# Kernel optimization log

Hardware: AMD Instinct MI355X
Metric: run time of the kernel (lower is better)

The kernel has to match this reference:

```python
import jax, jax.numpy as jnp
import numpy as np

IN_DIM, INTER_DIM, OUT_DIM = 512, 256, 512


def setup_inputs() -> dict:
    key = jax.random.key(0)
    k1, k2, k3, k4 = jax.random.split(key, 4)
    feat_map = jax.random.normal(k1, (8, IN_DIM, 64, 64), dtype=jnp.float32)
    # xavier-uniform-style init scales
    lim_p = float(np.sqrt(6.0 / (IN_DIM + INTER_DIM)))
    lim_w = float(np.sqrt(6.0 / (IN_DIM + OUT_DIM)))
    phi_w = jax.random.uniform(k2, (INTER_DIM, IN_DIM), jnp.float32, -lim_p, lim_p)
    theta_w = jax.random.uniform(k3, (INTER_DIM, IN_DIM), jnp.float32, -lim_p, lim_p)
    weight = jax.random.uniform(k4, (IN_DIM, OUT_DIM), jnp.float32, -lim_w, lim_w)
    return {"feat_map": feat_map, "phi_w": phi_w, "theta_w": theta_w, "weight": weight}


def reference(feat_map, phi_w, theta_w, weight):
    B, D, H, W = feat_map.shape
    # b c h w -> b (h w) c
    feat_vec = jnp.transpose(feat_map.reshape(B, D, H * W), (0, 2, 1))  # [B, HW, D]
    phi = jnp.einsum('bnc,ic->bni', feat_vec, phi_w)      # [B, HW, inter]
    theta = jnp.einsum('bnc,ic->bni', feat_vec, theta_w)  # [B, HW, inter]
    product = jnp.einsum('bni,bmi->bnm', phi, theta)      # [B, HW, HW]
    phi_norm = jnp.linalg.norm(phi, axis=-1, keepdims=True)      # [B, HW, 1]
    theta_norm = jnp.linalg.norm(theta, axis=-1, keepdims=True)  # [B, HW, 1]
    norms = phi_norm * jnp.transpose(theta_norm, (0, 2, 1))      # [B, HW, HW]
    sim = jax.nn.softmax(product / norms, axis=-1)
    out = jnp.einsum('bnm,bmc->bnc', sim, feat_vec)  # [B, HW, D]
    out = jnp.einsum('bnc,cd->bnd', out, weight)     # [B, HW, out_dim]
    # b (h w) d -> b d h w
    updated = jnp.transpose(out, (0, 2, 1)).reshape(B, -1, H, W)
    return jax.nn.relu(updated)
```

## Files before the change

kernel.cpp:

```cpp
#include <hip/hip_runtime.h>


typedef short s8v __attribute__((ext_vector_type(8)));
typedef float f4v __attribute__((ext_vector_type(4)));

__device__ inline ushort f2bf(float x) {
  union { float f; unsigned u; } v; v.f = x;
  unsigned u = v.u + 0x7fff + ((v.u >> 16) & 1);
  return (ushort)(u >> 16);
}

__global__ __launch_bounds__(256) void k0a(const float* __restrict__ feat,
                                           ushort* __restrict__ featT,
                                           ushort* __restrict__ featV) {
  int bid = blockIdx.x;
  int b = bid >> 9, cb = (bid >> 6) & 7, mt = bid & 63;
  int t = threadIdx.x;
  __shared__ ushort tile[64][72];

#pragma unroll
  for (int p = 0; p < 4; p++) {
    int ci = p * 16 + (t >> 4);
    int mi = (t & 15) * 4;
    float4 v = *(const float4*)&feat[((size_t)(b * 512 + cb * 64 + ci)) * 4096 + mt * 64 + mi];
    ushort4 u; u.x = f2bf(v.x); u.y = f2bf(v.y); u.z = f2bf(v.z); u.w = f2bf(v.w);
    *(ushort4*)&featV[((size_t)(b * 64 + mt) * 512 + cb * 64 + ci) * 64 + mi] = u;
    tile[ci][mi] = u.x; tile[ci][mi + 1] = u.y; tile[ci][mi + 2] = u.z; tile[ci][mi + 3] = u.w;
  }
  __syncthreads();
  int m = t >> 2, cs = (t & 3) * 16;
  ushort tmp[16];
#pragma unroll
  for (int j = 0; j < 16; j++) tmp[j] = tile[cs + j][m];
  ushort* dst = &featT[((size_t)(b * 4096 + mt * 64 + m)) * 512 + cb * 64 + cs];
  *(s8v*)dst = *(s8v*)&tmp[0];
  *(s8v*)(dst + 8) = *(s8v*)&tmp[8];
}

__global__ __launch_bounds__(256) void k0b(const float* __restrict__ pw,
                                           const float* __restrict__ tw,
                                           ushort* __restrict__ wbp,
                                           ushort* __restrict__ wbt) {
  int bid = blockIdx.x;
  const float* src = (bid < 128) ? pw : tw;
  ushort* dst = (bid < 128) ? wbp : wbt;
  int idx = ((bid & 127) * 256 + threadIdx.x) * 4;
  float4 v = *(const float4*)&src[idx];
  ushort4 u; u.x = f2bf(v.x); u.y = f2bf(v.y); u.z = f2bf(v.z); u.w = f2bf(v.w);
  *(ushort4*)&dst[idx] = u;
}

__global__ __launch_bounds__(256) void k0c(const float* __restrict__ w,
                                           ushort* __restrict__ wT) {
  int bid = blockIdx.x;
  int cb = bid >> 3, db = bid & 7;
  int t = threadIdx.x;
  __shared__ ushort tile[64][72];
#pragma unroll
  for (int p = 0; p < 4; p++) {
    int ci = p * 16 + (t >> 4);
    int di = (t & 15) * 4;
    float4 v = *(const float4*)&w[(size_t)(cb * 64 + ci) * 512 + db * 64 + di];
    tile[ci][di] = f2bf(v.x); tile[ci][di + 1] = f2bf(v.y);
    tile[ci][di + 2] = f2bf(v.z); tile[ci][di + 3] = f2bf(v.w);
  }
  __syncthreads();
  int d = t >> 2, cs = (t & 3) * 16;
  ushort tmp[16];
#pragma unroll
  for (int j = 0; j < 16; j++) tmp[j] = tile[cs + j][d];
  ushort* dst = &wT[(size_t)(db * 64 + d) * 512 + cb * 64 + cs];
  *(s8v*)dst = *(s8v*)&tmp[0];
  *(s8v*)(dst + 8) = *(s8v*)&tmp[8];
}

__global__ __launch_bounds__(512) void k1_gemm(
    const ushort* __restrict__ featT, const ushort* __restrict__ wbp,
    const ushort* __restrict__ wbt, ushort* __restrict__ phi_n,
    ushort* __restrict__ theta_n) {
  int bid = blockIdx.x;
  int b = bid & 7;
  int rest = bid >> 3;
  int half = rest & 1;
  int nt = rest >> 1;
  const ushort* wb = half ? wbt : wbp;
  ushort* dst = half ? theta_n : phi_n;
  int t = threadIdx.x;
  int lane = t & 63, w = t >> 6;
  int col = lane & 15, quad = lane >> 4;
  int n0 = nt * 128;

  const ushort* abase =
      featT + ((size_t)(b * 4096 + n0 + w * 16 + col)) * 512 + quad * 8;

  f4v acc[16];
#pragma unroll
  for (int i = 0; i < 16; i++) acc[i] = (f4v){0.f, 0.f, 0.f, 0.f};

#pragma unroll 2
  for (int kc = 0; kc < 16; kc++) {
    s8v a = *(const s8v*)(abase + kc * 32);
#pragma unroll
    for (int it = 0; it < 16; it++) {
      s8v bf = *(const s8v*)(wb + (size_t)(it * 16 + col) * 512 + kc * 32 + quad * 8);
      acc[it] = __builtin_amdgcn_mfma_f32_16x16x32_bf16(a, bf, acc[it], 0, 0, 0);
    }
  }
  float rinv[4];
#pragma unroll
  for (int reg = 0; reg < 4; reg++) {
    float ss = 0.f;
#pragma unroll
    for (int it = 0; it < 16; it++) ss += acc[it][reg] * acc[it][reg];
    ss += __shfl_xor(ss, 1); ss += __shfl_xor(ss, 2);
    ss += __shfl_xor(ss, 4); ss += __shfl_xor(ss, 8);
    rinv[reg] = rsqrtf(ss);
  }
#pragma unroll
  for (int it = 0; it < 16; it++) {
#pragma unroll
    for (int reg = 0; reg < 4; reg++) {
      dst[((size_t)(b * 4096 + n0 + w * 16 + quad * 4 + reg)) * 256 + it * 16 + col] =
          f2bf(acc[it][reg] * rinv[reg]);
    }
  }
}

__global__ __launch_bounds__(512, 2) void k3_attn(
    const ushort* __restrict__ phi_n, const ushort* __restrict__ theta_n,
    const ushort* __restrict__ featV, ushort* __restrict__ out1) {
  int bid = blockIdx.x;
  int b = bid & 7;
  int n0 = (bid >> 3) << 6;
  int t = threadIdx.x;
  int lane = t & 63, w = t >> 6;
  int col = lane & 15, quad = lane >> 4;
  int mh4 = w & 3, rh = w >> 2;
  int l32 = lane & 31, h32 = lane >> 5;
  int cs = col & 7;

  __shared__ __align__(16) ushort ks[2 * 16384];
  __shared__ __align__(16) ushort ps[2 * 4096];
  __shared__ float dred[4 * 64];

  s8v qfA[8], qfB[8];
  {
    const ushort* qa = phi_n + ((size_t)(b * 4096 + n0 + rh * 32 + col)) * 256 + quad * 8;
#pragma unroll
    for (int f = 0; f < 8; f++) qfA[f] = *(const s8v*)(qa + f * 32);
    const ushort* qb = qa + 16 * 256;
#pragma unroll
    for (int f = 0; f < 8; f++) qfB[f] = *(const s8v*)(qb + f * 32);
  }

  const ushort* thb = theta_n + (size_t)b * 4096 * 256;
  const ushort* vbb = featV + (size_t)b * 64 * 512 * 64 + (size_t)(w * 64) * 64;

  f4v acc[16];
#pragma unroll
  for (int i = 0; i < 16; i++) acc[i] = (f4v){0.f, 0.f, 0.f, 0.f};
  float denp[8] = {0.f, 0.f, 0.f, 0.f, 0.f, 0.f, 0.f, 0.f};

#pragma unroll
  for (int u = 0; u < 4; u++) {
    int row = w * 8 + u * 2 + h32;
    s8v val = *(const s8v*)(thb + (size_t)row * 256 + l32 * 8);
    *(s8v*)(ks + row * 256 + ((l32 ^ (row & 7)) * 8)) = val;
  }
  __syncthreads();

#pragma unroll 1
  for (int mt = 0; mt < 64; mt++) {
    const ushort* kc_ = ks + (mt & 1) * 16384;
    ushort* kn_ = ks + ((mt & 1) ^ 1) * 16384;
    ushort* pw_ = ps + (mt & 1) * 4096;

    s8v kreg[4];
    if (mt < 63) {
      int m1 = (mt + 1) << 6;
#pragma unroll
      for (int u = 0; u < 4; u++) {
        int row = w * 8 + u * 2 + h32;
        kreg[u] = *(const s8v*)(thb + (size_t)(m1 + row) * 256 + l32 * 8);
      }
    }
    s8v v0[4], v1[4];
    {
      const ushort* vb = vbb + (size_t)mt * 32768;
#pragma unroll
      for (int ct = 0; ct < 4; ct++) {
        const ushort* p = vb + (ct * 16 + col) * 64 + quad * 8;
        v0[ct] = *(const s8v*)p;
        v1[ct] = *(const s8v*)(p + 32);
      }
    }

    f4v svA = (f4v){0.f, 0.f, 0.f, 0.f};
    f4v svB = (f4v){0.f, 0.f, 0.f, 0.f};
    {
      const ushort* kb = kc_ + (mh4 * 16 + col) * 256;
      __builtin_amdgcn_s_setprio(1);
#pragma unroll
      for (int kk = 0; kk < 8; kk++) {
        int pos = ((kk * 4 + quad) ^ cs) * 8;
        s8v bf = *(const s8v*)(kb + pos);
        svA = __builtin_amdgcn_mfma_f32_16x16x32_bf16(qfA[kk], bf, svA, 0, 0, 0);
        svB = __builtin_amdgcn_mfma_f32_16x16x32_bf16(qfB[kk], bf, svB, 0, 0, 0);
      }
      __builtin_amdgcn_s_setprio(0);
    }

    float pA[4], pB[4];
#pragma unroll
    for (int r = 0; r < 4; r++) {
      pA[r] = __expf(svA[r]);
      pB[r] = __expf(svB[r]);
      denp[r] += pA[r];
      denp[4 + r] += pB[r];
    }

    {
      int j0 = mh4 * 2 + (col >> 3);
#pragma unroll
      for (int r = 0; r < 4; r++) {
        int nA = rh * 32 + quad * 4 + r;
        pw_[nA * 64 + ((j0 ^ (nA & 7)) * 8) + cs] = f2bf(pA[r]);
        int nB = nA + 16;
        pw_[nB * 64 + ((j0 ^ (nB & 7)) * 8) + cs] = f2bf(pB[r]);
      }
    }
    if (mt < 63) {
#pragma unroll
      for (int u = 0; u < 4; u++) {
        int row = w * 8 + u * 2 + h32;
        *(s8v*)(kn_ + row * 256 + ((l32 ^ (row & 7)) * 8)) = kreg[u];
      }
    }
    __syncthreads();

    __builtin_amdgcn_s_setprio(1);
#pragma unroll
    for (int rs = 0; rs < 4; rs++) {
      const ushort* pb = pw_ + (rs * 16 + col) * 64;
      s8v pf0 = *(const s8v*)(pb + ((quad ^ cs) * 8));
      s8v pf1 = *(const s8v*)(pb + (((quad + 4) ^ cs) * 8));
#pragma unroll
      for (int ct = 0; ct < 4; ct++) {
        acc[rs * 4 + ct] =
            __builtin_amdgcn_mfma_f32_16x16x32_bf16(pf0, v0[ct], acc[rs * 4 + ct], 0, 0, 0);
        acc[rs * 4 + ct] =
            __builtin_amdgcn_mfma_f32_16x16x32_bf16(pf1, v1[ct], acc[rs * 4 + ct], 0, 0, 0);
      }
    }
    __builtin_amdgcn_s_setprio(0);
  }

#pragma unroll
  for (int i = 0; i < 8; i++) {
    float d = denp[i];
    d += __shfl_xor(d, 1); d += __shfl_xor(d, 2);
    d += __shfl_xor(d, 4); d += __shfl_xor(d, 8);
    denp[i] = d;
  }
  if (col == 0) {
#pragma unroll
    for (int i = 0; i < 8; i++) {
      int n = rh * 32 + (i >> 2) * 16 + quad * 4 + (i & 3);
      dred[mh4 * 64 + n] = denp[i];
    }
  }
  __syncthreads();
  if (t < 64) dred[t] = 1.0f / (dred[t] + dred[64 + t] + dred[128 + t] + dred[192 + t]);
  __syncthreads();

#pragma unroll
  for (int rs = 0; rs < 4; rs++) {
#pragma unroll
    for (int ct = 0; ct < 4; ct++) {
#pragma unroll
      for (int reg = 0; reg < 4; reg++) {
        int n = rs * 16 + quad * 4 + reg;
        out1[((size_t)(b * 4096 + n0 + n)) * 512 + w * 64 + ct * 16 + col] =
            f2bf(acc[rs * 4 + ct][reg] * dred[n]);
      }
    }
  }
}

__global__ __launch_bounds__(512) void k4_out(
    const ushort* __restrict__ out1, const ushort* __restrict__ wT,
    float* __restrict__ out) {
  int bid = blockIdx.x;
  int b = bid & 7;
  int rest = bid >> 3;
  int dt = rest & 3;
  int nt = rest >> 2;
  int t = threadIdx.x;
  int lane = t & 63, w = t >> 6;
  int col = lane & 15, quad = lane >> 4;
  int dw = w & 1, nw = w >> 1;
  int d0 = dt * 128 + dw * 64;
  int n0 = nt * 256 + nw * 64;

  f4v acc[16];
#pragma unroll
  for (int i = 0; i < 16; i++) acc[i] = (f4v){0.f, 0.f, 0.f, 0.f};

#pragma unroll 2
  for (int kc = 0; kc < 16; kc++) {
    s8v af[4], bf[4];
#pragma unroll
    for (int rs = 0; rs < 4; rs++)
      af[rs] = *(const s8v*)(wT + (size_t)(d0 + rs * 16 + col) * 512 + kc * 32 + quad * 8);
#pragma unroll
    for (int ct = 0; ct < 4; ct++)
      bf[ct] = *(const s8v*)(out1 + ((size_t)(b * 4096 + n0 + ct * 16 + col)) * 512 +
                             kc * 32 + quad * 8);
#pragma unroll
    for (int rs = 0; rs < 4; rs++)
#pragma unroll
      for (int ct = 0; ct < 4; ct++)
        acc[rs * 4 + ct] =
            __builtin_amdgcn_mfma_f32_16x16x32_bf16(af[rs], bf[ct], acc[rs * 4 + ct], 0, 0, 0);
  }
#pragma unroll
  for (int rs = 0; rs < 4; rs++) {
#pragma unroll
    for (int ct = 0; ct < 4; ct++) {
#pragma unroll
      for (int reg = 0; reg < 4; reg++) {
        int d = d0 + rs * 16 + quad * 4 + reg;
        int n = n0 + ct * 16 + col;
        out[((size_t)(b * 512 + d)) * 4096 + n] = fmaxf(acc[rs * 4 + ct][reg], 0.f);
      }
    }
  }
}

extern "C" void kernel_launch(void* const* d_in, const int* in_sizes, int n_in,
                              void* d_out, int out_size, void* d_ws, size_t ws_size,
                              hipStream_t stream) {
  const float* feat    = (const float*)d_in[0];
  const float* phi_w   = (const float*)d_in[1];
  const float* theta_w = (const float*)d_in[2];
  const float* weight  = (const float*)d_in[3];
  float* out = (float*)d_out;

  ushort* wsu = (ushort*)d_ws;
  ushort* featT   = wsu;
  ushort* featV   = wsu + 16777216;
  ushort* phi_n   = wsu + 33554432;
  ushort* theta_n = wsu + 41943040;
  ushort* wbp     = wsu + 50331648;
  ushort* wbt     = wsu + 50462720;
  ushort* weightT = wsu + 50593792;
  ushort* out1    = wsu;

  k0a<<<dim3(4096), dim3(256), 0, stream>>>(feat, featT, featV);
  k0b<<<dim3(256), dim3(256), 0, stream>>>(phi_w, theta_w, wbp, wbt);
  k0c<<<dim3(64), dim3(256), 0, stream>>>(weight, weightT);
  k1_gemm<<<dim3(512), dim3(512), 0, stream>>>(featT, wbp, wbt, phi_n, theta_n);
  k3_attn<<<dim3(512), dim3(512), 0, stream>>>(phi_n, theta_n, featV, out1);
  k4_out<<<dim3(512), dim3(512), 0, stream>>>(out1, weightT, out);
}
```

Baseline: 599.6 us.

## Split attention kernel work across 16 waves per block instead of 8

The attention kernel moves from 512 to 1024 threads per block. Each wave now handles 16 query rows and 32 output channels instead of 32 and 64. The QK dot product is split into two independent accumulator chains over halves of the inner dimension, then summed before the exponential. The goal is more resident waves and shorter per-wave dependency chains to hide latency. In exchange, each K fragment is reused by fewer MFMAs and P is read from LDS by twice as many waves, so LDS traffic grows.

```diff
diff --git a/kernel.cpp b/kernel.cpp
--- a/kernel.cpp
+++ b/kernel.cpp
@@ -126,7 +126,7 @@
   }
 }
 
-__global__ __launch_bounds__(512, 2) void k3_attn(
+__global__ __launch_bounds__(1024, 4) void k3_attn(
     const ushort* __restrict__ phi_n, const ushort* __restrict__ theta_n,
     const ushort* __restrict__ featV, ushort* __restrict__ out1) {
   int bid = blockIdx.x;
@@ -135,7 +135,7 @@
   int t = threadIdx.x;
   int lane = t & 63, w = t >> 6;
   int col = lane & 15, quad = lane >> 4;
-  int mh4 = w & 3, rh = w >> 2;
+  int mh4 = w & 3, rq = w >> 2;
   int l32 = lane & 31, h32 = lane >> 5;
   int cs = col & 7;
 
@@ -143,27 +143,24 @@
   __shared__ __align__(16) ushort ps[2 * 4096];
   __shared__ float dred[4 * 64];
 
-  s8v qfA[8], qfB[8];
+  s8v qf[8];
   {
-    const ushort* qa = phi_n + ((size_t)(b * 4096 + n0 + rh * 32 + col)) * 256 + quad * 8;
-#pragma unroll
-    for (int f = 0; f < 8; f++) qfA[f] = *(const s8v*)(qa + f * 32);
-    const ushort* qb = qa + 16 * 256;
-#pragma unroll
-    for (int f = 0; f < 8; f++) qfB[f] = *(const s8v*)(qb + f * 32);
+    const ushort* qa = phi_n + ((size_t)(b * 4096 + n0 + rq * 16 + col)) * 256 + quad * 8;
+#pragma unroll
+    for (int f = 0; f < 8; f++) qf[f] = *(const s8v*)(qa + f * 32);
   }
 
   const ushort* thb = theta_n + (size_t)b * 4096 * 256;
-  const ushort* vbb = featV + (size_t)b * 64 * 512 * 64 + (size_t)(w * 64) * 64;
-
-  f4v acc[16];
-#pragma unroll
-  for (int i = 0; i < 16; i++) acc[i] = (f4v){0.f, 0.f, 0.f, 0.f};
-  float denp[8] = {0.f, 0.f, 0.f, 0.f, 0.f, 0.f, 0.f, 0.f};
-
-#pragma unroll
-  for (int u = 0; u < 4; u++) {
-    int row = w * 8 + u * 2 + h32;
+  const ushort* vbb = featV + (size_t)b * 64 * 512 * 64 + (size_t)(w * 32) * 64;
+
+  f4v acc[8];
+#pragma unroll
+  for (int i = 0; i < 8; i++) acc[i] = (f4v){0.f, 0.f, 0.f, 0.f};
+  float denp[4] = {0.f, 0.f, 0.f, 0.f};
+
+#pragma unroll
+  for (int u = 0; u < 2; u++) {
+    int row = w * 4 + u * 2 + h32;
     s8v val = *(const s8v*)(thb + (size_t)row * 256 + l32 * 8);
     *(s8v*)(ks + row * 256 + ((l32 ^ (row & 7)) * 8)) = val;
   }
@@ -175,64 +172,62 @@
     ushort* kn_ = ks + ((mt & 1) ^ 1) * 16384;
     ushort* pw_ = ps + (mt & 1) * 4096;
 
-    s8v kreg[4];
+    s8v kreg[2];
     if (mt < 63) {
       int m1 = (mt + 1) << 6;
 #pragma unroll
-      for (int u = 0; u < 4; u++) {
-        int row = w * 8 + u * 2 + h32;
+      for (int u = 0; u < 2; u++) {
+        int row = w * 4 + u * 2 + h32;
         kreg[u] = *(const s8v*)(thb + (size_t)(m1 + row) * 256 + l32 * 8);
       }
     }
-    s8v v0[4], v1[4];
+    s8v v0[2], v1[2];
     {
       const ushort* vb = vbb + (size_t)mt * 32768;
 #pragma unroll
-      for (int ct = 0; ct < 4; ct++) {
+      for (int ct = 0; ct < 2; ct++) {
         const ushort* p = vb + (ct * 16 + col) * 64 + quad * 8;
         v0[ct] = *(const s8v*)p;
         v1[ct] = *(const s8v*)(p + 32);
       }
     }
 
-    f4v svA = (f4v){0.f, 0.f, 0.f, 0.f};
-    f4v svB = (f4v){0.f, 0.f, 0.f, 0.f};
+    f4v sv0 = (f4v){0.f, 0.f, 0.f, 0.f};
+    f4v sv1 = (f4v){0.f, 0.f, 0.f, 0.f};
     {
       const ushort* kb = kc_ + (mh4 * 16 + col) * 256;
       __builtin_amdgcn_s_setprio(1);
 #pragma unroll
-      for (int kk = 0; kk < 8; kk++) {
-        int pos = ((kk * 4 + quad) ^ cs) * 8;
-        s8v bf = *(const s8v*)(kb + pos);
-        svA = __builtin_amdgcn_mfma_f32_16x16x32_bf16(qfA[kk], bf, svA, 0, 0, 0);
-        svB = __builtin_amdgcn_mfma_f32_16x16x32_bf16(qfB[kk], bf, svB, 0, 0, 0);
+      for (int kk = 0; kk < 4; kk++) {
+        int pos0 = ((kk * 4 + quad) ^ cs) * 8;
+        int pos1 = (((kk + 4) * 4 + quad) ^ cs) * 8;
+        s8v b0 = *(const s8v*)(kb + pos0);
+        s8v b1 = *(const s8v*)(kb + pos1);
+        sv0 = __builtin_amdgcn_mfma_f32_16x16x32_bf16(qf[kk], b0, sv0, 0, 0, 0);
+        sv1 = __builtin_amdgcn_mfma_f32_16x16x32_bf16(qf[kk + 4], b1, sv1, 0, 0, 0);
       }
       __builtin_amdgcn_s_setprio(0);
     }
 
-    float pA[4], pB[4];
+    float pA[4];
 #pragma unroll
     for (int r = 0; r < 4; r++) {
-      pA[r] = __expf(svA[r]);
-      pB[r] = __expf(svB[r]);
+      pA[r] = __expf(sv0[r] + sv1[r]);
       denp[r] += pA[r];
-      denp[4 + r] += pB[r];
     }
 
     {
       int j0 = mh4 * 2 + (col >> 3);
 #pragma unroll
       for (int r = 0; r < 4; r++) {
-        int nA = rh * 32 + quad * 4 + r;
-        pw_[nA * 64 + ((j0 ^ (nA & 7)) * 8) + cs] = f2bf(pA[r]);
-        int nB = nA + 16;
-        pw_[nB * 64 + ((j0 ^ (nB & 7)) * 8) + cs] = f2bf(pB[r]);
+        int n = rq * 16 + quad * 4 + r;
+        pw_[n * 64 + ((j0 ^ (n & 7)) * 8) + cs] = f2bf(pA[r]);
       }
     }
     if (mt < 63) {
 #pragma unroll
-      for (int u = 0; u < 4; u++) {
-        int row = w * 8 + u * 2 + h32;
+      for (int u = 0; u < 2; u++) {
+        int row = w * 4 + u * 2 + h32;
         *(s8v*)(kn_ + row * 256 + ((l32 ^ (row & 7)) * 8)) = kreg[u];
       }
     }
@@ -245,29 +240,26 @@
       s8v pf0 = *(const s8v*)(pb + ((quad ^ cs) * 8));
       s8v pf1 = *(const s8v*)(pb + (((quad + 4) ^ cs) * 8));
 #pragma unroll
-      for (int ct = 0; ct < 4; ct++) {
-        acc[rs * 4 + ct] =
-            __builtin_amdgcn_mfma_f32_16x16x32_bf16(pf0, v0[ct], acc[rs * 4 + ct], 0, 0, 0);
-        acc[rs * 4 + ct] =
-            __builtin_amdgcn_mfma_f32_16x16x32_bf16(pf1, v1[ct], acc[rs * 4 + ct], 0, 0, 0);
+      for (int ct = 0; ct < 2; ct++) {
+        acc[rs * 2 + ct] =
+            __builtin_amdgcn_mfma_f32_16x16x32_bf16(pf0, v0[ct], acc[rs * 2 + ct], 0, 0, 0);
+        acc[rs * 2 + ct] =
+            __builtin_amdgcn_mfma_f32_16x16x32_bf16(pf1, v1[ct], acc[rs * 2 + ct], 0, 0, 0);
       }
     }
     __builtin_amdgcn_s_setprio(0);
   }
 
 #pragma unroll
-  for (int i = 0; i < 8; i++) {
-    float d = denp[i];
+  for (int r = 0; r < 4; r++) {
+    float d = denp[r];
     d += __shfl_xor(d, 1); d += __shfl_xor(d, 2);
     d += __shfl_xor(d, 4); d += __shfl_xor(d, 8);
-    denp[i] = d;
+    denp[r] = d;
   }
   if (col == 0) {
 #pragma unroll
-    for (int i = 0; i < 8; i++) {
-      int n = rh * 32 + (i >> 2) * 16 + quad * 4 + (i & 3);
-      dred[mh4 * 64 + n] = denp[i];
-    }
+    for (int r = 0; r < 4; r++) dred[mh4 * 64 + rq * 16 + quad * 4 + r] = denp[r];
   }
   __syncthreads();
   if (t < 64) dred[t] = 1.0f / (dred[t] + dred[64 + t] + dred[128 + t] + dred[192 + t]);
@@ -276,12 +268,12 @@
 #pragma unroll
   for (int rs = 0; rs < 4; rs++) {
 #pragma unroll
-    for (int ct = 0; ct < 4; ct++) {
+    for (int ct = 0; ct < 2; ct++) {
 #pragma unroll
       for (int reg = 0; reg < 4; reg++) {
         int n = rs * 16 + quad * 4 + reg;
-        out1[((size_t)(b * 4096 + n0 + n)) * 512 + w * 64 + ct * 16 + col] =
-            f2bf(acc[rs * 4 + ct][reg] * dred[n]);
+        out1[((size_t)(b * 4096 + n0 + n)) * 512 + w * 32 + ct * 16 + col] =
+            f2bf(acc[rs * 2 + ct][reg] * dred[n]);
       }
     }
   }
@@ -360,6 +352,6 @@
   k0b<<<dim3(256), dim3(256), 0, stream>>>(phi_w, theta_w, wbp, wbt);
   k0c<<<dim3(64), dim3(256), 0, stream>>>(weight, weightT);
   k1_gemm<<<dim3(512), dim3(512), 0, stream>>>(featT, wbp, wbt, phi_n, theta_n);
-  k3_attn<<<dim3(512), dim3(512), 0, stream>>>(phi_n, theta_n, featV, out1);
+  k3_attn<<<dim3(512), dim3(1024), 0, stream>>>(phi_n, theta_n, featV, out1);
   k4_out<<<dim3(512), dim3(512), 0, stream>>>(out1, weightT, out);
 }
```

Result: slower. 851.8 us (+42.1%).

## Retile projection GEMM into 64x64 warp tiles with cross-warp norm reduction

Applied to the files above, without the earlier changes.

Each warp in the phi/theta projection GEMM used to compute 16 rows by all 256 output columns, loading one A fragment and 16 B fragments per k-step. It now computes a 64x64 tile (4 row subtiles by 4 column subtiles), loading 4 A and 4 B fragments per k-step, which cuts global/L2 traffic per MFMA. Because a row's columns are now split across 4 warps, the row L2 norm is reduced through a shared-memory partial-sum array plus a __syncthreads. This adds shared memory and a barrier, and the stores stay scattered 2-byte writes.

```diff
diff --git a/kernel.cpp b/kernel.cpp
--- a/kernel.cpp
+++ b/kernel.cpp
@@ -88,10 +88,13 @@
   int t = threadIdx.x;
   int lane = t & 63, w = t >> 6;
   int col = lane & 15, quad = lane >> 4;
-  int n0 = nt * 128;
-
-  const ushort* abase =
-      featT + ((size_t)(b * 4096 + n0 + w * 16 + col)) * 512 + quad * 8;
+  int wn = w >> 2, wi = w & 3;
+  int nb = nt * 128 + wn * 64;
+
+  __shared__ float part[128][4];
+
+  const ushort* ab = featT + ((size_t)(b * 4096 + nb + col)) * 512 + quad * 8;
+  const ushort* bb = wb + ((size_t)(wi * 64 + col)) * 512 + quad * 8;
 
   f4v acc[16];
 #pragma unroll
@@ -99,29 +102,57 @@
 
 #pragma unroll 2
   for (int kc = 0; kc < 16; kc++) {
-    s8v a = *(const s8v*)(abase + kc * 32);
-#pragma unroll
-    for (int it = 0; it < 16; it++) {
-      s8v bf = *(const s8v*)(wb + (size_t)(it * 16 + col) * 512 + kc * 32 + quad * 8);
-      acc[it] = __builtin_amdgcn_mfma_f32_16x16x32_bf16(a, bf, acc[it], 0, 0, 0);
-    }
-  }
-  float rinv[4];
-#pragma unroll
-  for (int reg = 0; reg < 4; reg++) {
-    float ss = 0.f;
-#pragma unroll
-    for (int it = 0; it < 16; it++) ss += acc[it][reg] * acc[it][reg];
-    ss += __shfl_xor(ss, 1); ss += __shfl_xor(ss, 2);
-    ss += __shfl_xor(ss, 4); ss += __shfl_xor(ss, 8);
-    rinv[reg] = rsqrtf(ss);
-  }
-#pragma unroll
-  for (int it = 0; it < 16; it++) {
+    s8v af[4], bf[4];
+#pragma unroll
+    for (int rs = 0; rs < 4; rs++)
+      af[rs] = *(const s8v*)(ab + (size_t)(rs * 16) * 512 + kc * 32);
+#pragma unroll
+    for (int ct = 0; ct < 4; ct++)
+      bf[ct] = *(const s8v*)(bb + (size_t)(ct * 16) * 512 + kc * 32);
+#pragma unroll
+    for (int rs = 0; rs < 4; rs++)
+#pragma unroll
+      for (int ct = 0; ct < 4; ct++)
+        acc[rs * 4 + ct] =
+            __builtin_amdgcn_mfma_f32_16x16x32_bf16(af[rs], bf[ct], acc[rs * 4 + ct], 0, 0, 0);
+  }
+
+#pragma unroll
+  for (int rs = 0; rs < 4; rs++) {
 #pragma unroll
     for (int reg = 0; reg < 4; reg++) {
-      dst[((size_t)(b * 4096 + n0 + w * 16 + quad * 4 + reg)) * 256 + it * 16 + col] =
-          f2bf(acc[it][reg] * rinv[reg]);
+      float ss = 0.f;
+#pragma unroll
+      for (int ct = 0; ct < 4; ct++) {
+        float v = acc[rs * 4 + ct][reg];
+        ss += v * v;
+      }
+      ss += __shfl_xor(ss, 1); ss += __shfl_xor(ss, 2);
+      ss += __shfl_xor(ss, 4); ss += __shfl_xor(ss, 8);
+      if (col == 0) part[wn * 64 + rs * 16 + quad * 4 + reg][wi] = ss;
+    }
+  }
+  __syncthreads();
+
+  float rinv[4][4];
+#pragma unroll
+  for (int rs = 0; rs < 4; rs++) {
+#pragma unroll
+    for (int reg = 0; reg < 4; reg++) {
+      float4 p = *(const float4*)&part[wn * 64 + rs * 16 + quad * 4 + reg][0];
+      rinv[rs][reg] = rsqrtf(p.x + p.y + p.z + p.w);
+    }
+  }
+
+#pragma unroll
+  for (int rs = 0; rs < 4; rs++) {
+#pragma unroll
+    for (int ct = 0; ct < 4; ct++) {
+#pragma unroll
+      for (int reg = 0; reg < 4; reg++) {
+        dst[((size_t)(b * 4096 + nb + rs * 16 + quad * 4 + reg)) * 256 +
+            wi * 64 + ct * 16 + col] = f2bf(acc[rs * 4 + ct][reg] * rinv[rs][reg]);
+      }
     }
   }
 }
```

Result: faster. 540.3 us (-9.9%).
